# Optimization experiments

Measured on AMD Instinct MI355X. Metric: run time of the kernel, lower is better.

Reference implementation:

```python
import jax, jax.numpy as jnp
import numpy as np

B, M, V, E, D, T = 512, 64, 20000, 1024, 384, 100
EPS = 1e-5


def setup_inputs() -> dict:
    key = jax.random.key(0)
    ks = jax.random.split(key, 26)
    w = lambda k, shape: (jax.random.normal(k, shape, jnp.float32) * 0.02)
    return {
        'x': jax.random.uniform(ks[0], (B, V), jnp.float32),
        'emb': jax.random.normal(ks[1], (B, M, D), jnp.float32),
        'lengths': jax.random.randint(ks[2], (B,), 1, M + 1, jnp.int32),
        'fc11_w': w(ks[3], (E, V)), 'fc11_b': jnp.zeros((E,), jnp.float32),
        'fc12_w': w(ks[4], (E, E)), 'fc12_b': jnp.zeros((E,), jnp.float32),
        'q_w': w(ks[5], (D, E)), 'q_b': jnp.zeros((D,), jnp.float32),
        'k_w': w(ks[6], (D, D)), 'k_b': jnp.zeros((D,), jnp.float32),
        'v_w': w(ks[7], (D, D)), 'v_b': jnp.zeros((D,), jnp.float32),
        'mean_w': w(ks[8], (T, D)), 'mean_b': jnp.zeros((T,), jnp.float32),
        'logvar_w': w(ks[9], (T, D)), 'logvar_b': jnp.zeros((T,), jnp.float32),
        'mean_bn_b': jnp.zeros((T,), jnp.float32),
        'logvar_bn_b': jnp.zeros((T,), jnp.float32),
        'dec_w': w(ks[10], (V, T)), 'dec_b': jnp.zeros((V,), jnp.float32),
        'dec_bn_b': jnp.zeros((V,), jnp.float32),
    }


def _bn(h, bias):
    # BatchNorm1d, training-mode batch stats, weight frozen at 1 (requires_grad=False)
    mu = h.mean(axis=0)
    var = h.var(axis=0)  # biased variance, as torch BN normalization
    return (h - mu) / jnp.sqrt(var + EPS) + bias


def reference(x, emb, lengths, fc11_w, fc11_b, fc12_w, fc12_b,
              q_w, q_b, k_w, k_b, v_w, v_b,
              mean_w, mean_b, logvar_w, logvar_b,
              mean_bn_b, logvar_bn_b, dec_w, dec_b, dec_bn_b):
    # encoder MLP (dropout p=0 -> identity)
    e1 = jax.nn.softplus(x @ fc11_w.T + fc11_b)
    h_bow = jax.nn.softplus(e1 @ fc12_w.T + fc12_b)  # [B, E]

    # ragged single-query attention over sentence embeddings, vectorized
    q = h_bow @ q_w.T + q_b                              # [B, D]
    k = jnp.einsum('bmd,ed->bme', emb, k_w) + k_b        # [B, M, D]
    v = jnp.einsum('bmd,ed->bme', emb, v_w) + v_b        # [B, M, D]
    scores = jnp.einsum('bd,bmd->bm', q, k) / jnp.sqrt(jnp.float32(D))
    valid = jnp.arange(M)[None, :] < lengths[:, None]    # [B, M]
    scores = jnp.where(valid, scores, -jnp.inf)
    alpha = jax.nn.softmax(scores, axis=-1)
    d_i = jnp.einsum('bm,bmd->bd', alpha, v)             # [B, D]

    mu = _bn(d_i @ mean_w.T + mean_b, mean_bn_b)         # [B, T]
    logvar = _bn(d_i @ logvar_w.T + logvar_b, logvar_bn_b)
    z = mu  # eval-mode reparameterize
    theta = jax.nn.softmax(z, axis=1)

    logit = theta @ dec_w.T + dec_b
    recon_log = jax.nn.log_softmax(_bn(logit, dec_bn_b), axis=-1)
    recon_loss = -(x * recon_log).sum(axis=1).mean()

    # KL prior: a = ones -> mu2 = 0, var2 = 1 - 1/T (scalar)
    var2 = 1.0 - 1.0 / T
    var = jnp.exp(logvar)
    kld = 0.5 * ((var / var2 + mu * mu / var2 + jnp.log(var2) - logvar).sum(axis=1) - T)
    loss_kl = kld.mean()
    return recon_loss + loss_kl
```

## Files before the change

kernel.cpp:

```cpp
#include <hip/hip_runtime.h>
#include <cstddef>

#define NB 512
#define NM 64
#define NV 20000
#define NE 1024
#define ND 384
#define NT 100
#define EPS 1e-5f

#define NVP 20096
#define NKP 128
#define NHS 256

typedef __bf16 bf16x8 __attribute__((ext_vector_type(8)));
typedef float f32x4 __attribute__((ext_vector_type(4)));

__device__ __forceinline__ float softplus_f(float x) {
    return fmaxf(x, 0.f) + log1pf(expf(-fabsf(x)));
}

__device__ __forceinline__ unsigned short f2bf(float f) {
    unsigned u = __builtin_bit_cast(unsigned, f);
    unsigned r = u + 0x7FFFu + ((u >> 16) & 1u);
    return (unsigned short)(r >> 16);
}

__device__ __forceinline__ float bf2f(unsigned short u) {
    return __builtin_bit_cast(float, (unsigned)u << 16);
}

__device__ __forceinline__ uint4 pack_bf8(float4 a, float4 b) {
    union { unsigned short u[8]; uint4 v; } r;
    r.u[0] = f2bf(a.x); r.u[1] = f2bf(a.y); r.u[2] = f2bf(a.z); r.u[3] = f2bf(a.w);
    r.u[4] = f2bf(b.x); r.u[5] = f2bf(b.y); r.u[6] = f2bf(b.z); r.u[7] = f2bf(b.w);
    return r.v;
}

__device__ __forceinline__ void convert8(const float* __restrict__ s,
                                         unsigned short* __restrict__ d,
                                         int b, int tid) {
    const size_t i = ((size_t)b * 256 + tid) * 8;
    const float4 a = *reinterpret_cast<const float4*>(s + i);
    const float4 c = *reinterpret_cast<const float4*>(s + i + 4);
    *reinterpret_cast<uint4*>(d + i) = pack_bf8(a, c);
}

#define PREP_C12 512
#define PREP_QW  192
#define PREP_VW  72
#define PREP_TR  144
#define PREP_HD  257
#define PREP_DW  (NVP / 2)
#define PREP_BLOCKS (PREP_C12 + PREP_QW + PREP_VW + PREP_TR + PREP_HD + PREP_DW)

__global__ __launch_bounds__(256) void prep_kernel(
        const float* __restrict__ fc12_w, unsigned short* __restrict__ w12b,
        const float* __restrict__ q_w,    unsigned short* __restrict__ qwb,
        const float* __restrict__ v_w,    unsigned short* __restrict__ vwb,
        const float* __restrict__ k_w,    unsigned short* __restrict__ kTb,
        const float* __restrict__ mw, const float* __restrict__ lw,
        const float* __restrict__ mb, const float* __restrict__ lb,
        unsigned short* __restrict__ headwb, float* __restrict__ headbb,
        const float* __restrict__ dec_w,  unsigned short* __restrict__ decwb) {
    __shared__ float tile[32][33];
    int b = blockIdx.x;
    const int tid = threadIdx.x;
    if (b < PREP_C12) { convert8(fc12_w, w12b, b, tid); return; }
    b -= PREP_C12;
    if (b < PREP_QW) { convert8(q_w, qwb, b, tid); return; }
    b -= PREP_QW;
    if (b < PREP_VW) { convert8(v_w, vwb, b, tid); return; }
    b -= PREP_VW;
    if (b < PREP_TR) {
        const int bx = (b % 12) * 32, by = (b / 12) * 32;
        const int tx = tid & 31, ty = tid >> 5;
        #pragma unroll
        for (int i = 0; i < 4; ++i)
            tile[ty + 8 * i][tx] = k_w[(size_t)(by + ty + 8 * i) * ND + bx + tx];
        __syncthreads();
        #pragma unroll
        for (int i = 0; i < 4; ++i)
            kTb[(size_t)(bx + ty + 8 * i) * ND + by + tx] = f2bf(tile[tx][ty + 8 * i]);
        return;
    }
    b -= PREP_TR;
    if (b < PREP_HD) {
        if (b == NHS) {
            if (tid < NHS)
                headbb[tid] = (tid < NT) ? mb[tid]
                            : (tid >= 128 && tid < 128 + NT) ? lb[tid - 128] : 0.f;
            return;
        }
        const float* src = (b < NT) ? (mw + (size_t)b * ND)
                         : (b >= 128 && b < 128 + NT) ? (lw + (size_t)(b - 128) * ND) : nullptr;
        for (int c = tid; c < ND; c += 256)
            headwb[(size_t)b * ND + c] = src ? f2bf(src[c]) : (unsigned short)0;
        return;
    }
    b -= PREP_HD;
    {
        const int n = b * 2 + (tid >> 7);
        const int k = tid & 127;
        decwb[(size_t)n * NKP + k] =
            (n < NV && k < NT) ? f2bf(dec_w[(size_t)n * NT + k]) : (unsigned short)0;
    }
}

#define BM 128
#define BN 128
#define BK 32

__global__ __launch_bounds__(256) void gemm_f32_splitk(
        const float* __restrict__ A,
        const float* __restrict__ Bw,
        unsigned short* __restrict__ partial,
        int M, int N, int K, int S, int steps_total, int gx, int gy) {
    __shared__ __align__(16) unsigned short Asl[BM * BK];
    __shared__ __align__(16) unsigned short Bsl[BN * BK];
    const int tid = threadIdx.x;
    const int l = blockIdx.x >> 3;
    const int xcd = blockIdx.x & 7;
    const int bm = l % gy;
    const int rest = l / gy;
    const int bn = rest % gx;
    const int s_loc = rest / gx;
    const int s = xcd * (S >> 3) + s_loc;

    const int row0 = bm * BM, col0 = bn * BN;
    const int k_begin = (int)(((long)s * steps_total) / S) * BK;
    const int k_end   = (int)(((long)(s + 1) * steps_total) / S) * BK;

    const int sr = tid >> 2;
    const int sc = (tid & 3) * 8;
    const int wave = tid >> 6, lane = tid & 63;
    const int wm = wave >> 1, wn = wave & 1;
    const int lrow = lane & 15, lkb = lane >> 4;

    f32x4 acc[4][4] = {};
    const float* Ab = A + (size_t)row0 * K;
    const float* Bb = Bw + (size_t)col0 * K;

    for (int k0 = k_begin; k0 < k_end; k0 += BK) {
        float4 ra[2][2], rb[2][2];
        #pragma unroll
        for (int h = 0; h < 2; ++h) {
            const float* pa = Ab + (size_t)(h * 64 + sr) * K + k0 + sc;
            const float* pb = Bb + (size_t)(h * 64 + sr) * K + k0 + sc;
            ra[h][0] = *reinterpret_cast<const float4*>(pa);
            ra[h][1] = *reinterpret_cast<const float4*>(pa + 4);
            rb[h][0] = *reinterpret_cast<const float4*>(pb);
            rb[h][1] = *reinterpret_cast<const float4*>(pb + 4);
        }
        __syncthreads();
        #pragma unroll
        for (int h = 0; h < 2; ++h) {
            *reinterpret_cast<uint4*>(&Asl[(h * 64 + sr) * BK + sc]) = pack_bf8(ra[h][0], ra[h][1]);
            *reinterpret_cast<uint4*>(&Bsl[(h * 64 + sr) * BK + sc]) = pack_bf8(rb[h][0], rb[h][1]);
        }
        __syncthreads();
        bf16x8 af[4], bfr[4];
        #pragma unroll
        for (int i = 0; i < 4; ++i) {
            af[i]  = *reinterpret_cast<const bf16x8*>(&Asl[(wm * 64 + i * 16 + lrow) * BK + lkb * 8]);
            bfr[i] = *reinterpret_cast<const bf16x8*>(&Bsl[(wn * 64 + i * 16 + lrow) * BK + lkb * 8]);
        }
        #pragma unroll
        for (int i = 0; i < 4; ++i)
            #pragma unroll
            for (int j = 0; j < 4; ++j)
                acc[i][j] = __builtin_amdgcn_mfma_f32_16x16x32_bf16(af[i], bfr[j], acc[i][j], 0, 0, 0);
    }

    unsigned short* P = partial + (size_t)s * M * N;
    #pragma unroll
    for (int i = 0; i < 4; ++i) {
        const int rbase = row0 + wm * 64 + i * 16 + lkb * 4;
        #pragma unroll
        for (int j = 0; j < 4; ++j) {
            const int col = col0 + wn * 64 + j * 16 + lrow;
            #pragma unroll
            for (int r = 0; r < 4; ++r)
                P[(size_t)(rbase + r) * N + col] = f2bf(acc[i][j][r]);
        }
    }
}

__global__ __launch_bounds__(256) void gemm_mfma_splitk(
        const unsigned short* __restrict__ A,
        const unsigned short* __restrict__ Bw,
        unsigned short* __restrict__ partial,
        int M, int N, int K, int S, int steps_total) {
    __shared__ __align__(16) unsigned short Asl[BM * BK];
    __shared__ __align__(16) unsigned short Bsl[BN * BK];
    const int tid = threadIdx.x;
    const int bn = blockIdx.x, bm = blockIdx.y, s = blockIdx.z;
    const int row0 = bm * BM, col0 = bn * BN;
    const int k_begin = (int)(((long)s * steps_total) / S) * BK;
    const int k_end   = (int)(((long)(s + 1) * steps_total) / S) * BK;

    const int srow = tid >> 2;
    const int scol = (tid & 3) * 8;
    const int wave = tid >> 6, lane = tid & 63;
    const int wm = wave >> 1, wn = wave & 1;
    const int lrow = lane & 15, lkb = lane >> 4;

    f32x4 acc[4][4] = {};
    const unsigned short* Ab = A + (size_t)row0 * K;
    const unsigned short* Bb = Bw + (size_t)col0 * K;

    for (int k0 = k_begin; k0 < k_end; k0 += BK) {
        #pragma unroll
        for (int i = 0; i < 2; ++i) {
            const int r = i * 64 + srow;
            __builtin_amdgcn_global_load_lds(
                (const __attribute__((address_space(1))) void*)(Ab + (size_t)r * K + k0 + scol),
                (__attribute__((address_space(3))) void*)(&Asl[(i * 256 + tid) * 8]),
                16, 0, 0);
            __builtin_amdgcn_global_load_lds(
                (const __attribute__((address_space(1))) void*)(Bb + (size_t)r * K + k0 + scol),
                (__attribute__((address_space(3))) void*)(&Bsl[(i * 256 + tid) * 8]),
                16, 0, 0);
        }
        __syncthreads();
        bf16x8 af[4], bfr[4];
        #pragma unroll
        for (int i = 0; i < 4; ++i) {
            af[i]  = *reinterpret_cast<const bf16x8*>(&Asl[(wm * 64 + i * 16 + lrow) * BK + lkb * 8]);
            bfr[i] = *reinterpret_cast<const bf16x8*>(&Bsl[(wn * 64 + i * 16 + lrow) * BK + lkb * 8]);
        }
        #pragma unroll
        for (int i = 0; i < 4; ++i)
            #pragma unroll
            for (int j = 0; j < 4; ++j)
                acc[i][j] = __builtin_amdgcn_mfma_f32_16x16x32_bf16(af[i], bfr[j], acc[i][j], 0, 0, 0);
        __syncthreads();
    }

    unsigned short* P = partial + (size_t)s * M * N;
    #pragma unroll
    for (int i = 0; i < 4; ++i) {
        const int rbase = row0 + wm * 64 + i * 16 + lkb * 4;
        #pragma unroll
        for (int j = 0; j < 4; ++j) {
            const int col = col0 + wn * 64 + j * 16 + lrow;
            #pragma unroll
            for (int r = 0; r < 4; ++r)
                P[(size_t)(rbase + r) * N + col] = f2bf(acc[i][j][r]);
        }
    }
}

__global__ __launch_bounds__(256) void gemm64_splitk(
        const unsigned short* __restrict__ A,
        const unsigned short* __restrict__ Bw,
        unsigned short* __restrict__ partial,
        int M, int N, int K, int S, int steps_total) {
    __shared__ __align__(16) unsigned short Asl[64 * BK];
    __shared__ __align__(16) unsigned short Bsl[64 * BK];
    const int tid = threadIdx.x;
    const int bn = blockIdx.x, bm = blockIdx.y, s = blockIdx.z;
    const int row0 = bm * 64, col0 = bn * 64;
    const int k_begin = (int)(((long)s * steps_total) / S) * BK;
    const int k_end   = (int)(((long)(s + 1) * steps_total) / S) * BK;

    const int srow = tid >> 2;
    const int scol = (tid & 3) * 8;
    const int wave = tid >> 6, lane = tid & 63;
    const int wm = wave >> 1, wn = wave & 1;
    const int lrow = lane & 15, lkb = lane >> 4;

    f32x4 acc[2][2] = {};
    const unsigned short* Ab = A + (size_t)row0 * K;
    const unsigned short* Bb = Bw + (size_t)col0 * K;

    for (int k0 = k_begin; k0 < k_end; k0 += BK) {
        __builtin_amdgcn_global_load_lds(
            (const __attribute__((address_space(1))) void*)(Ab + (size_t)srow * K + k0 + scol),
            (__attribute__((address_space(3))) void*)(&Asl[tid * 8]),
            16, 0, 0);
        __builtin_amdgcn_global_load_lds(
            (const __attribute__((address_space(1))) void*)(Bb + (size_t)srow * K + k0 + scol),
            (__attribute__((address_space(3))) void*)(&Bsl[tid * 8]),
            16, 0, 0);
        __syncthreads();
        bf16x8 af[2], bfr[2];
        #pragma unroll
        for (int i = 0; i < 2; ++i) {
            af[i]  = *reinterpret_cast<const bf16x8*>(&Asl[(wm * 32 + i * 16 + lrow) * BK + lkb * 8]);
            bfr[i] = *reinterpret_cast<const bf16x8*>(&Bsl[(wn * 32 + i * 16 + lrow) * BK + lkb * 8]);
        }
        #pragma unroll
        for (int i = 0; i < 2; ++i)
            #pragma unroll
            for (int j = 0; j < 2; ++j)
                acc[i][j] = __builtin_amdgcn_mfma_f32_16x16x32_bf16(af[i], bfr[j], acc[i][j], 0, 0, 0);
        __syncthreads();
    }

    unsigned short* P = partial + (size_t)s * M * N;
    #pragma unroll
    for (int i = 0; i < 2; ++i) {
        const int rbase = row0 + wm * 32 + i * 16 + lkb * 4;
        #pragma unroll
        for (int j = 0; j < 2; ++j) {
            const int col = col0 + wn * 32 + j * 16 + lrow;
            #pragma unroll
            for (int r = 0; r < 4; ++r)
                P[(size_t)(rbase + r) * N + col] = f2bf(acc[i][j][r]);
        }
    }
}

template<int OUT_BF16, int ACT, int HASBIAS>
__global__ __launch_bounds__(256) void reduce_splitk_bf(
        const unsigned short* __restrict__ partial,
        const float* __restrict__ bias,
        void* __restrict__ out, int MN, int N, int S) {
    const int i0 = (blockIdx.x * 256 + threadIdx.x) * 8;
    if (i0 >= MN) return;
    float sum[8] = {};
    for (int s = 0; s < S; ++s) {
        union { uint4 v; unsigned short u[8]; } p;
        p.v = *reinterpret_cast<const uint4*>(partial + (size_t)s * MN + i0);
        #pragma unroll
        for (int j = 0; j < 8; ++j) sum[j] += bf2f(p.u[j]);
    }
    if (HASBIAS) {
        const int nb = i0 % N;
        #pragma unroll
        for (int j = 0; j < 8; ++j) sum[j] += bias[nb + j];
    }
    if (ACT) {
        #pragma unroll
        for (int j = 0; j < 8; ++j) sum[j] = softplus_f(sum[j]);
    }
    if (OUT_BF16) {
        union { uint4 v; unsigned short u[8]; } r;
        #pragma unroll
        for (int j = 0; j < 8; ++j) r.u[j] = f2bf(sum[j]);
        *reinterpret_cast<uint4*>((unsigned short*)out + i0) = r.v;
    } else {
        float* o = (float*)out + i0;
        *reinterpret_cast<float4*>(o)     = make_float4(sum[0], sum[1], sum[2], sum[3]);
        *reinterpret_cast<float4*>(o + 4) = make_float4(sum[4], sum[5], sum[6], sum[7]);
    }
}

template<int OUT_BF16, int ACT, int HASBIAS, int COLSTATS>
__global__ __launch_bounds__(256) void gemm_mfma(
        const unsigned short* __restrict__ A,
        const unsigned short* __restrict__ Bw,
        const float* __restrict__ bias,
        void* __restrict__ Cout,
        float* __restrict__ colp,
        int M, int Nout, int K) {
    __shared__ __align__(16) unsigned short Asl[BM * BK];
    __shared__ __align__(16) unsigned short Bsl[BN * BK];
    const int tid = threadIdx.x;
    const int row0 = blockIdx.y * BM, col0 = blockIdx.x * BN;
    const int srow = tid >> 2;
    const int scol = (tid & 3) * 8;
    const int wave = tid >> 6, lane = tid & 63;
    const int wm = wave >> 1, wn = wave & 1;
    const int lrow = lane & 15, lkb = lane >> 4;

    f32x4 acc[4][4] = {};
    const unsigned short* Ab = A + (size_t)row0 * K;
    const unsigned short* Bb = Bw + (size_t)col0 * K;

    for (int k0 = 0; k0 < K; k0 += BK) {
        #pragma unroll
        for (int i = 0; i < 2; ++i) {
            const int r = i * 64 + srow;
            __builtin_amdgcn_global_load_lds(
                (const __attribute__((address_space(1))) void*)(Ab + (size_t)r * K + k0 + scol),
                (__attribute__((address_space(3))) void*)(&Asl[(i * 256 + tid) * 8]),
                16, 0, 0);
            __builtin_amdgcn_global_load_lds(
                (const __attribute__((address_space(1))) void*)(Bb + (size_t)r * K + k0 + scol),
                (__attribute__((address_space(3))) void*)(&Bsl[(i * 256 + tid) * 8]),
                16, 0, 0);
        }
        __syncthreads();
        bf16x8 af[4], bfr[4];
        #pragma unroll
        for (int i = 0; i < 4; ++i) {
            af[i]  = *reinterpret_cast<const bf16x8*>(&Asl[(wm * 64 + i * 16 + lrow) * BK + lkb * 8]);
            bfr[i] = *reinterpret_cast<const bf16x8*>(&Bsl[(wn * 64 + i * 16 + lrow) * BK + lkb * 8]);
        }
        #pragma unroll
        for (int i = 0; i < 4; ++i)
            #pragma unroll
            for (int j = 0; j < 4; ++j)
                acc[i][j] = __builtin_amdgcn_mfma_f32_16x16x32_bf16(af[i], bfr[j], acc[i][j], 0, 0, 0);
        __syncthreads();
    }

    #pragma unroll
    for (int j = 0; j < 4; ++j) {
        const int col = col0 + wn * 64 + j * 16 + lrow;
        const bool cok = col < Nout;
        const float bv = HASBIAS ? (cok ? bias[col] : 0.f) : 0.f;
        float csum = 0.f, csq = 0.f;
        #pragma unroll
        for (int i = 0; i < 4; ++i) {
            const int rbase = row0 + wm * 64 + i * 16 + lkb * 4;
            #pragma unroll
            for (int r = 0; r < 4; ++r) {
                float v = acc[i][j][r] + bv;
                if (ACT == 1) v = softplus_f(v);
                if (COLSTATS) { csum += v; csq = fmaf(v, v, csq); }
                if (cok) {
                    if (OUT_BF16)
                        ((unsigned short*)Cout)[(size_t)(rbase + r) * Nout + col] = f2bf(v);
                    else
                        ((float*)Cout)[(size_t)(rbase + r) * Nout + col] = v;
                }
            }
        }
        if (COLSTATS) {
            csum += __shfl_xor(csum, 16); csum += __shfl_xor(csum, 32);
            csq  += __shfl_xor(csq, 16);  csq  += __shfl_xor(csq, 32);
            if (lkb == 0) {
                const int w8 = blockIdx.y * 2 + wm;
                colp[(size_t)w8 * NVP + col] = csum;
                colp[(size_t)(8 + w8) * NVP + col] = csq;
            }
        }
    }
}

__global__ __launch_bounds__(256) void attn_kernel(const unsigned short* __restrict__ qkp,
                                                   const float* __restrict__ emb,
                                                   const int* __restrict__ lengths,
                                                   unsigned short* __restrict__ cb) {
    const int b = blockIdx.x;
    const int tid = threadIdx.x;
    __shared__ unsigned short es[NM * ND];
    __shared__ float qs[ND];
    __shared__ float sc[NM];

    const float* ebase = emb + (size_t)b * NM * ND;
    for (int i = tid; i < NM * ND / 4; i += 256) {
        const float4 v = *reinterpret_cast<const float4*>(ebase + (size_t)i * 4);
        ushort4 o;
        o.x = f2bf(v.x); o.y = f2bf(v.y); o.z = f2bf(v.z); o.w = f2bf(v.w);
        *reinterpret_cast<ushort4*>(&es[i * 4]) = o;
    }
    for (int d = tid; d < ND; d += 256) {
        float acc = 0.f;
        #pragma unroll
        for (int s = 0; s < 8; ++s)
            acc += bf2f(qkp[((size_t)s * NB + b) * ND + d]);
        qs[d] = acc;
    }
    __syncthreads();

    const int wave = tid >> 6, lane = tid & 63;
    const float scale = 0.05103103630798288f;

    for (int m = wave; m < NM; m += 4) {
        float s = 0.f;
        for (int d = lane; d < ND; d += 64) s = fmaf(bf2f(es[m * ND + d]), qs[d], s);
        #pragma unroll
        for (int off = 32; off; off >>= 1) s += __shfl_xor(s, off);
        if (lane == 0) sc[m] = s * scale;
    }
    __syncthreads();

    const int len = lengths[b];
    if (tid < 64) {
        float s = (tid < len) ? sc[tid] : -INFINITY;
        float mx = s;
        #pragma unroll
        for (int off = 32; off; off >>= 1) mx = fmaxf(mx, __shfl_xor(mx, off));
        float e = (tid < len) ? expf(s - mx) : 0.f;
        float sum = e;
        #pragma unroll
        for (int off = 32; off; off >>= 1) sum += __shfl_xor(sum, off);
        sc[tid] = e / sum;
    }
    __syncthreads();

    for (int d = tid; d < ND; d += 256) {
        float acc = 0.f;
        for (int m = 0; m < len; ++m) acc = fmaf(sc[m], bf2f(es[m * ND + d]), acc);
        cb[(size_t)b * ND + d] = f2bf(acc);
    }
}

__global__ __launch_bounds__(256) void bn_batch(const float* __restrict__ hl,
                                                const float* __restrict__ mbnb,
                                                const float* __restrict__ lbnb,
                                                float* __restrict__ mu,
                                                float* __restrict__ lv) {
    const int t = blockIdx.x;
    const int sel = blockIdx.y;
    const int col = sel ? 128 + t : t;
    const float* bnb = sel ? lbnb : mbnb;
    float* dst = sel ? lv : mu;
    const int tid = threadIdx.x;

    float s = 0.f, ss = 0.f;
    for (int b = tid; b < NB; b += 256) {
        const float v = hl[(size_t)b * NHS + col];
        s += v; ss += v * v;
    }
    __shared__ float rs[256], rss[256];
    rs[tid] = s; rss[tid] = ss;
    __syncthreads();
    for (int off = 128; off; off >>= 1) {
        if (tid < off) { rs[tid] += rs[tid + off]; rss[tid] += rss[tid + off]; }
        __syncthreads();
    }
    const float mean = rs[0] / (float)NB;
    const float var = rss[0] / (float)NB - mean * mean;
    const float rstd = rsqrtf(var + EPS);
    const float bb = bnb[t];
    for (int b = tid; b < NB; b += 256) {
        dst[(size_t)b * NT + t] = (hl[(size_t)b * NHS + col] - mean) * rstd + bb;
    }
}

__global__ __launch_bounds__(128) void theta_kl(const float* __restrict__ mu,
                                                const float* __restrict__ lv,
                                                unsigned short* __restrict__ thetab,
                                                float* __restrict__ kld_p) {
    const int b = blockIdx.x, tid = threadIdx.x;
    const float var2 = 1.0f - 1.0f / (float)NT;
    const float inv_var2 = 1.0f / var2;
    __shared__ float red[128];

    const float m = (tid < NT) ? mu[(size_t)b * NT + tid] : -INFINITY;
    red[tid] = m;
    __syncthreads();
    for (int off = 64; off; off >>= 1) {
        if (tid < off) red[tid] = fmaxf(red[tid], red[tid + off]);
        __syncthreads();
    }
    const float mx = red[0];
    __syncthreads();

    const float e = (tid < NT) ? expf(m - mx) : 0.f;
    red[tid] = e;
    __syncthreads();
    for (int off = 64; off; off >>= 1) {
        if (tid < off) red[tid] += red[tid + off];
        __syncthreads();
    }
    const float sum = red[0];
    __syncthreads();
    thetab[(size_t)b * NKP + tid] = (tid < NT) ? f2bf(e / sum) : (unsigned short)0;

    float term = 0.f;
    if (tid < NT) {
        const float l = lv[(size_t)b * NT + tid];
        term = expf(l) * inv_var2 + m * m * inv_var2 - l;
    }
    red[tid] = term;
    __syncthreads();
    for (int off = 64; off; off >>= 1) {
        if (tid < off) red[tid] += red[tid + off];
        __syncthreads();
    }
    if (tid == 0)
        kld_p[b] = 0.5f * (red[0] + (float)NT * logf(var2) - (float)NT);
}

__global__ __launch_bounds__(256) void stats_final(const float* __restrict__ colp,
                                                   float* __restrict__ cmu,
                                                   float* __restrict__ crstd) {
    const int v = blockIdx.x * 256 + threadIdx.x;
    if (v >= NV) return;
    float s = 0.f, q = 0.f;
    #pragma unroll
    for (int w = 0; w < 8; ++w) {
        s += colp[(size_t)w * NVP + v];
        q += colp[(size_t)(8 + w) * NVP + v];
    }
    const float mean = s / (float)NB;
    cmu[v] = mean;
    crstd[v] = rsqrtf(q / (float)NB - mean * mean + EPS);
}

__global__ __launch_bounds__(256) void row_recon(const unsigned short* __restrict__ logitb,
                                                 const float* __restrict__ x,
                                                 const float* __restrict__ cmu,
                                                 const float* __restrict__ crstd,
                                                 const float* __restrict__ dbnb,
                                                 float* __restrict__ recon_p) {
    const int b = blockIdx.x, tid = threadIdx.x;
    const unsigned short* lr = logitb + (size_t)b * NV;
    const float* xr = x + (size_t)b * NV;

    float m_i = -INFINITY, s_i = 0.f, xz = 0.f, xs = 0.f;
    for (int v = tid * 8; v < NV; v += 2048) {
        union { uint4 v4; unsigned short u[8]; } lw;
        lw.v4 = *reinterpret_cast<const uint4*>(lr + v);
        const float4 x0 = *reinterpret_cast<const float4*>(xr + v);
        const float4 x1 = *reinterpret_cast<const float4*>(xr + v + 4);
        const float4 c0 = *reinterpret_cast<const float4*>(cmu + v);
        const float4 c1 = *reinterpret_cast<const float4*>(cmu + v + 4);
        const float4 r0 = *reinterpret_cast<const float4*>(crstd + v);
        const float4 r1 = *reinterpret_cast<const float4*>(crstd + v + 4);
        const float4 d0 = *reinterpret_cast<const float4*>(dbnb + v);
        const float4 d1 = *reinterpret_cast<const float4*>(dbnb + v + 4);
        const float xv[8] = {x0.x,x0.y,x0.z,x0.w,x1.x,x1.y,x1.z,x1.w};
        const float cm[8] = {c0.x,c0.y,c0.z,c0.w,c1.x,c1.y,c1.z,c1.w};
        const float cr[8] = {r0.x,r0.y,r0.z,r0.w,r1.x,r1.y,r1.z,r1.w};
        const float db[8] = {d0.x,d0.y,d0.z,d0.w,d1.x,d1.y,d1.z,d1.w};
        float z[8];
        #pragma unroll
        for (int j = 0; j < 8; ++j)
            z[j] = fmaf(bf2f(lw.u[j]) - cm[j], cr[j], db[j]);
        float mx = z[0];
        #pragma unroll
        for (int j = 1; j < 8; ++j) mx = fmaxf(mx, z[j]);
        const float mnew = fmaxf(m_i, mx);
        float e8 = 0.f;
        #pragma unroll
        for (int j = 0; j < 8; ++j) e8 += expf(z[j] - mnew);
        s_i = s_i * expf(m_i - mnew) + e8;
        m_i = mnew;
        #pragma unroll
        for (int j = 0; j < 8; ++j) {
            xz = fmaf(xv[j], z[j], xz);
            xs += xv[j];
        }
    }

    __shared__ float rm[256], rs[256], rxz[256], rxs[256];
    rm[tid] = m_i; rs[tid] = s_i; rxz[tid] = xz; rxs[tid] = xs;
    __syncthreads();
    for (int off = 128; off; off >>= 1) {
        if (tid < off) {
            const float m1 = rm[tid], m2 = rm[tid + off];
            const float s1 = rs[tid], s2 = rs[tid + off];
            const float mm = fmaxf(m1, m2);
            rm[tid] = mm;
            rs[tid] = s1 * expf(m1 - mm) + s2 * expf(m2 - mm);
            rxz[tid] += rxz[tid + off];
            rxs[tid] += rxs[tid + off];
        }
        __syncthreads();
    }
    if (tid == 0) {
        const float lse = rm[0] + logf(rs[0]);
        recon_p[b] = rxz[0] - lse * rxs[0];
    }
}

__global__ __launch_bounds__(512) void finalize(const float* __restrict__ recon_p,
                                                const float* __restrict__ kld_p,
                                                float* __restrict__ out) {
    const int tid = threadIdx.x;
    __shared__ float r1[512], r2[512];
    r1[tid] = recon_p[tid];
    r2[tid] = kld_p[tid];
    __syncthreads();
    for (int off = 256; off; off >>= 1) {
        if (tid < off) { r1[tid] += r1[tid + off]; r2[tid] += r2[tid + off]; }
        __syncthreads();
    }
    if (tid == 0) out[0] = (-r1[0] + r2[0]) / (float)NB;
}

extern "C" void kernel_launch(void* const* d_in, const int* in_sizes, int n_in,
                              void* d_out, int out_size, void* d_ws, size_t ws_size,
                              hipStream_t stream) {
    const float* x       = (const float*)d_in[0];
    const float* emb     = (const float*)d_in[1];
    const int*   lengths = (const int*)d_in[2];
    const float* fc11_w  = (const float*)d_in[3];
    const float* fc11_b  = (const float*)d_in[4];
    const float* fc12_w  = (const float*)d_in[5];
    const float* fc12_b  = (const float*)d_in[6];
    const float* q_w     = (const float*)d_in[7];
    const float* q_b     = (const float*)d_in[8];
    const float* k_w     = (const float*)d_in[9];
    const float* v_w     = (const float*)d_in[11];
    const float* v_b     = (const float*)d_in[12];
    const float* mean_w  = (const float*)d_in[13];
    const float* mean_b  = (const float*)d_in[14];
    const float* lvw     = (const float*)d_in[15];
    const float* lvb     = (const float*)d_in[16];
    const float* mbnb    = (const float*)d_in[17];
    const float* lbnb    = (const float*)d_in[18];
    const float* dec_w   = (const float*)d_in[19];
    const float* dec_b   = (const float*)d_in[20];
    const float* dbnb    = (const float*)d_in[21];
    float* out = (float*)d_out;

    char* base = (char*)d_ws;
    size_t off = 0;
    auto alloc = [&](size_t bytes) -> void* {
        void* p = base + off;
        off += (bytes + 255) & ~(size_t)255;
        return p;
    };

    unsigned short* logitb = (unsigned short*)alloc((size_t)NB * NV * 2);
    unsigned short* w12b   = (unsigned short*)alloc((size_t)NE * NE * 2);
    unsigned short* e1b    = (unsigned short*)alloc((size_t)NB * NE * 2);
    unsigned short* hb     = (unsigned short*)alloc((size_t)NB * NE * 2);
    unsigned short* qwb    = (unsigned short*)alloc((size_t)ND * NE * 2);
    unsigned short* kTb    = (unsigned short*)alloc((size_t)ND * ND * 2);
    unsigned short* vwb    = (unsigned short*)alloc((size_t)ND * ND * 2);
    unsigned short* qb     = (unsigned short*)alloc((size_t)NB * ND * 2);
    unsigned short* cb     = (unsigned short*)alloc((size_t)NB * ND * 2);
    unsigned short* dib    = (unsigned short*)alloc((size_t)NB * ND * 2);
    unsigned short* headwb = (unsigned short*)alloc((size_t)NHS * ND * 2);
    float*          headbb = (float*)alloc((size_t)NHS * 4);
    float*          hl     = (float*)alloc((size_t)NB * NHS * 4);
    float*          mu     = (float*)alloc((size_t)NB * NT * 4);
    float*          lv     = (float*)alloc((size_t)NB * NT * 4);
    float*          colp   = (float*)alloc((size_t)16 * NVP * 4);
    float*          cmu    = (float*)alloc((size_t)NV * 4);
    float*          crstd  = (float*)alloc((size_t)NV * 4);
    float*          rp     = (float*)alloc((size_t)NB * 4);
    float*          kp     = (float*)alloc((size_t)NB * 4);
    unsigned short* decwb  = (unsigned short*)alloc((size_t)NVP * NKP * 2);
    unsigned short* thetab = (unsigned short*)alloc((size_t)NB * NKP * 2);
    unsigned short* smallp = (unsigned short*)alloc((size_t)16 * NB * ND * 2);
    const size_t part_bytes_per_s = ((size_t)NB * NE * 2 + 255) & ~(size_t)255;
    const size_t remain = (ws_size > off) ? (ws_size - off) : 0;
    const int S11 = (remain >= 32 * part_bytes_per_s) ? 32
                  : (remain >= 16 * part_bytes_per_s) ? 16 : 8;
    unsigned short* partb = (unsigned short*)alloc((size_t)S11 * NB * NE * 2);

    const dim3 blk(256);

    prep_kernel<<<PREP_BLOCKS, blk, 0, stream>>>(
        fc12_w, w12b, q_w, qwb, v_w, vwb, k_w, kTb,
        mean_w, lvw, mean_b, lvb, headwb, headbb, dec_w, decwb);

    gemm_f32_splitk<<<(NE / BN) * (NB / BM) * S11, blk, 0, stream>>>(
        x, fc11_w, partb, NB, NE, NV, S11, NV / BK, NE / BN, NB / BM);
    reduce_splitk_bf<1, 1, 1><<<(NB * NE) / 2048, blk, 0, stream>>>(
        partb, fc11_b, e1b, NB * NE, NE, S11);

    gemm_mfma_splitk<<<dim3(NE / BN, NB / BM, 8), blk, 0, stream>>>(
        e1b, w12b, partb, NB, NE, NE, 8, NE / BK);
    reduce_splitk_bf<1, 1, 1><<<(NB * NE) / 2048, blk, 0, stream>>>(
        partb, fc12_b, hb, NB * NE, NE, 8);

    gemm64_splitk<<<dim3(ND / 64, NB / 64, 16), blk, 0, stream>>>(
        hb, qwb, smallp, NB, ND, NE, 16, NE / BK);
    reduce_splitk_bf<1, 0, 1><<<(NB * ND) / 2048, blk, 0, stream>>>(
        smallp, q_b, qb, NB * ND, ND, 16);
    gemm64_splitk<<<dim3(ND / 64, NB / 64, 8), blk, 0, stream>>>(
        qb, kTb, smallp, NB, ND, ND, 8, ND / BK);
    attn_kernel<<<NB, 256, 0, stream>>>(smallp, emb, lengths, cb);
    gemm64_splitk<<<dim3(ND / 64, NB / 64, 8), blk, 0, stream>>>(
        cb, vwb, smallp, NB, ND, ND, 8, ND / BK);
    reduce_splitk_bf<1, 0, 1><<<(NB * ND) / 2048, blk, 0, stream>>>(
        smallp, v_b, dib, NB * ND, ND, 8);
    gemm64_splitk<<<dim3(NHS / 64, NB / 64, 8), blk, 0, stream>>>(
        dib, headwb, smallp, NB, NHS, ND, 8, ND / BK);
    reduce_splitk_bf<0, 0, 1><<<(NB * NHS) / 2048, blk, 0, stream>>>(
        smallp, headbb, hl, NB * NHS, NHS, 8);
    bn_batch<<<dim3(NT, 2), blk, 0, stream>>>(hl, mbnb, lbnb, mu, lv);
    theta_kl<<<NB, 128, 0, stream>>>(mu, lv, thetab, kp);
    gemm_mfma<1, 0, 1, 1><<<dim3(NVP / BN, NB / BM), blk, 0, stream>>>(
        thetab, decwb, dec_b, logitb, colp, NB, NV, NKP);
    stats_final<<<(NV + 255) / 256, blk, 0, stream>>>(colp, cmu, crstd);
    row_recon<<<NB, 256, 0, stream>>>(logitb, x, cmu, crstd, dbnb, rp);
    finalize<<<1, 512, 0, stream>>>(rp, kp, out);
}
```

Measured before the change: 195.5 us.

## Prefetch next K-tile into registers during MFMA and use native bf16 converts

```diff
diff --git a/kernel.cpp b/kernel.cpp
--- a/kernel.cpp
+++ b/kernel.cpp
@@ -31,10 +31,10 @@
 }
 
 __device__ __forceinline__ uint4 pack_bf8(float4 a, float4 b) {
-    union { unsigned short u[8]; uint4 v; } r;
-    r.u[0] = f2bf(a.x); r.u[1] = f2bf(a.y); r.u[2] = f2bf(a.z); r.u[3] = f2bf(a.w);
-    r.u[4] = f2bf(b.x); r.u[5] = f2bf(b.y); r.u[6] = f2bf(b.z); r.u[7] = f2bf(b.w);
-    return r.v;
+    bf16x8 v;
+    v[0] = (__bf16)a.x; v[1] = (__bf16)a.y; v[2] = (__bf16)a.z; v[3] = (__bf16)a.w;
+    v[4] = (__bf16)b.x; v[5] = (__bf16)b.y; v[6] = (__bf16)b.z; v[7] = (__bf16)b.w;
+    return __builtin_bit_cast(uint4, v);
 }
 
 __device__ __forceinline__ void convert8(const float* __restrict__ s,
@@ -130,6 +130,7 @@
     const int row0 = bm * BM, col0 = bn * BN;
     const int k_begin = (int)(((long)s * steps_total) / S) * BK;
     const int k_end   = (int)(((long)(s + 1) * steps_total) / S) * BK;
+    const int nsteps = (k_end - k_begin) / BK;
 
     const int sr = tid >> 2;
     const int sc = (tid & 3) * 8;
@@ -141,24 +142,40 @@
     const float* Ab = A + (size_t)row0 * K;
     const float* Bb = Bw + (size_t)col0 * K;
 
-    for (int k0 = k_begin; k0 < k_end; k0 += BK) {
-        float4 ra[2][2], rb[2][2];
-        #pragma unroll
-        for (int h = 0; h < 2; ++h) {
-            const float* pa = Ab + (size_t)(h * 64 + sr) * K + k0 + sc;
-            const float* pb = Bb + (size_t)(h * 64 + sr) * K + k0 + sc;
-            ra[h][0] = *reinterpret_cast<const float4*>(pa);
-            ra[h][1] = *reinterpret_cast<const float4*>(pa + 4);
-            rb[h][0] = *reinterpret_cast<const float4*>(pb);
-            rb[h][1] = *reinterpret_cast<const float4*>(pb + 4);
-        }
-        __syncthreads();
-        #pragma unroll
-        for (int h = 0; h < 2; ++h) {
-            *reinterpret_cast<uint4*>(&Asl[(h * 64 + sr) * BK + sc]) = pack_bf8(ra[h][0], ra[h][1]);
-            *reinterpret_cast<uint4*>(&Bsl[(h * 64 + sr) * BK + sc]) = pack_bf8(rb[h][0], rb[h][1]);
-        }
-        __syncthreads();
+    float4 ra[2][2], rb[2][2];
+
+#define LOADREGS(K0)                                                          \
+    {                                                                         \
+        _Pragma("unroll")                                                     \
+        for (int h = 0; h < 2; ++h) {                                         \
+            const float* pa = Ab + (size_t)(h * 64 + sr) * K + (K0) + sc;     \
+            const float* pb = Bb + (size_t)(h * 64 + sr) * K + (K0) + sc;     \
+            ra[h][0] = *reinterpret_cast<const float4*>(pa);                  \
+            ra[h][1] = *reinterpret_cast<const float4*>(pa + 4);              \
+            rb[h][0] = *reinterpret_cast<const float4*>(pb);                  \
+            rb[h][1] = *reinterpret_cast<const float4*>(pb + 4);              \
+        }                                                                     \
+    }
+
+#define WRITELDS()                                                            \
+    {                                                                         \
+        _Pragma("unroll")                                                     \
+        for (int h = 0; h < 2; ++h) {                                         \
+            *reinterpret_cast<uint4*>(&Asl[(h * 64 + sr) * BK + sc]) =        \
+                pack_bf8(ra[h][0], ra[h][1]);                                 \
+            *reinterpret_cast<uint4*>(&Bsl[(h * 64 + sr) * BK + sc]) =        \
+                pack_bf8(rb[h][0], rb[h][1]);                                 \
+        }                                                                     \
+    }
+
+    LOADREGS(k_begin);
+    WRITELDS();
+    __syncthreads();
+
+    for (int t = 0; t < nsteps; ++t) {
+        const bool has_next = (t + 1) < nsteps;
+        if (has_next) LOADREGS(k_begin + (t + 1) * BK);
+
         bf16x8 af[4], bfr[4];
         #pragma unroll
         for (int i = 0; i < 4; ++i) {
@@ -170,7 +187,13 @@
             #pragma unroll
             for (int j = 0; j < 4; ++j)
                 acc[i][j] = __builtin_amdgcn_mfma_f32_16x16x32_bf16(af[i], bfr[j], acc[i][j], 0, 0, 0);
-    }
+
+        __syncthreads();
+        if (has_next) WRITELDS();
+        __syncthreads();
+    }
+#undef LOADREGS
+#undef WRITELDS
 
     unsigned short* P = partial + (size_t)s * M * N;
     #pragma unroll
@@ -442,11 +465,10 @@
     __shared__ float sc[NM];
 
     const float* ebase = emb + (size_t)b * NM * ND;
-    for (int i = tid; i < NM * ND / 4; i += 256) {
-        const float4 v = *reinterpret_cast<const float4*>(ebase + (size_t)i * 4);
-        ushort4 o;
-        o.x = f2bf(v.x); o.y = f2bf(v.y); o.z = f2bf(v.z); o.w = f2bf(v.w);
-        *reinterpret_cast<ushort4*>(&es[i * 4]) = o;
+    for (int i = tid; i < NM * ND / 8; i += 256) {
+        const float4 v0 = *reinterpret_cast<const float4*>(ebase + (size_t)i * 8);
+        const float4 v1 = *reinterpret_cast<const float4*>(ebase + (size_t)i * 8 + 4);
+        *reinterpret_cast<uint4*>(&es[i * 8]) = pack_bf8(v0, v1);
     }
     for (int d = tid; d < ND; d += 256) {
         float acc = 0.f;
```

Measured after the change: 181.3 us. 7.3% less time.
